# Kernel tuning notes

Hardware: AMD Instinct MI355X
Metric: run time of the kernel (lower is better)

## Reference

```python
import jax, jax.numpy as jnp
import numpy as np

SIZE = 32          # resize target (self.size)
WIN = 11           # SSIM gaussian window
SIGMA = 1.5
THRESH = 0.3       # cal_thresh
C1 = (0.01 * 255.0) ** 2
C2 = (0.03 * 255.0) ** 2


def _gauss_kernel():
    x = jnp.arange(WIN, dtype=jnp.float32) - (WIN - 1) / 2.0
    g = jnp.exp(-(x ** 2) / (2.0 * SIGMA ** 2))
    g = g / g.sum()
    k = jnp.outer(g, g)
    return jnp.tile(k[None, None], (3, 1, 1, 1))  # [3,1,11,11] depthwise


def _dwconv(x, k):
    # x: [N,3,h,w] depthwise gaussian blur, SAME padding (pytorch-ssim style)
    return jax.lax.conv_general_dilated(x, k, (1, 1), 'SAME', feature_group_count=3)


def _crop_resize(img, box, H, W):
    # img [3,H,W], box cxcywh -> [3,SIZE,SIZE]; mimics int() crop + F.interpolate
    # (bilinear, align_corners=False)
    cx, cy, w, h = box[0], box[1], box[2], box[3]
    x0 = jnp.clip(jnp.floor(cx - w / 2), 0.0, W - 1.0)
    x1 = jnp.clip(jnp.floor(cx + w / 2), 0.0, float(W))
    y0 = jnp.clip(jnp.floor(cy - h / 2), 0.0, H - 1.0)
    y1 = jnp.clip(jnp.floor(cy + h / 2), 0.0, float(H))
    wp = jnp.maximum(x1 - x0, 1.0)  # crop width (>=1 to stay well-defined)
    hp = jnp.maximum(y1 - y0, 1.0)
    d = jnp.arange(SIZE, dtype=jnp.float32) + 0.5
    sx = x0 + jnp.clip(d * wp / SIZE - 0.5, 0.0, wp - 1.0)  # source cols
    sy = y0 + jnp.clip(d * hp / SIZE - 0.5, 0.0, hp - 1.0)  # source rows
    ix0 = jnp.floor(sx); iy0 = jnp.floor(sy)
    fx = sx - ix0; fy = sy - iy0
    ix0 = ix0.astype(jnp.int32); iy0 = iy0.astype(jnp.int32)
    ix1 = jnp.minimum(ix0 + 1, (x0 + wp - 1.0).astype(jnp.int32))
    iy1 = jnp.minimum(iy0 + 1, (y0 + hp - 1.0).astype(jnp.int32))

    def gat(iy, ix):
        return img[:, iy[:, None], ix[None, :]]  # [3,SIZE,SIZE]

    return (gat(iy0, ix0) * ((1 - fy)[None, :, None] * (1 - fx)[None, None, :])
            + gat(iy0, ix1) * ((1 - fy)[None, :, None] * fx[None, None, :])
            + gat(iy1, ix0) * (fy[None, :, None] * (1 - fx)[None, None, :])
            + gat(iy1, ix1) * (fy[None, :, None] * fx[None, None, :]))


def _pairwise_iou(gt, pr, eps=1e-16):
    # gt [B,Ng,4], pr [B,Np,4] cxcywh -> iou [B,Ng,Np] (same math as get_two_box_iou)
    g1, g2 = gt[:, :, None, :2], gt[:, :, None, 2:]
    p1, p2 = pr[:, None, :, :2], pr[:, None, :, 2:]
    tl = jnp.maximum(g1 - g2 / 2, p1 - p2 / 2)
    br = jnp.minimum(g1 + g2 / 2, p1 + p2 / 2)
    a_g = jnp.prod(gt[:, :, 2:], -1)[:, :, None]
    a_p = jnp.prod(pr[:, :, 2:], -1)[:, None, :]
    en = jnp.prod((tl < br).astype(gt.dtype), -1)
    a_i = jnp.prod(br - tl, -1) * en
    return a_i / (a_g + a_p - a_i + eps)


def _forward(imgs, gt_boxes, pred_boxes):
    B, C, H, W = imgs.shape
    Ng, Np = gt_boxes.shape[1], pred_boxes.shape[1]
    iou = _pairwise_iou(gt_boxes, pred_boxes)                        # [B,Ng,Np]
    valid = ((iou > THRESH)
             & (pred_boxes[:, None, :, 2] > 2)
             & (pred_boxes[:, None, :, 3] > 2))
    crop = jax.vmap(lambda im, bx: jax.vmap(lambda b: _crop_resize(im, b, H, W))(bx))
    g = crop(imgs, gt_boxes)    # [B,Ng,3,32,32]
    p = crop(imgs, pred_boxes)  # [B,Np,3,32,32]

    k = _gauss_kernel()
    mu_g = _dwconv(g.reshape(B * Ng, 3, SIZE, SIZE), k).reshape(B, Ng, 3, SIZE, SIZE)
    mu_p = _dwconv(p.reshape(B * Np, 3, SIZE, SIZE), k).reshape(B, Np, 3, SIZE, SIZE)
    sig_g = _dwconv((g * g).reshape(B * Ng, 3, SIZE, SIZE), k).reshape(B, Ng, 3, SIZE, SIZE) - mu_g ** 2
    sig_p = _dwconv((p * p).reshape(B * Np, 3, SIZE, SIZE), k).reshape(B, Np, 3, SIZE, SIZE) - mu_p ** 2

    gp = g[:, :, None] * p[:, None, :]                               # [B,Ng,Np,3,32,32]
    mug = mu_g[:, :, None]; mup = mu_p[:, None, :]
    sig_gp = _dwconv(gp.reshape(B * Ng * Np, 3, SIZE, SIZE), k).reshape(B, Ng, Np, 3, SIZE, SIZE) - mug * mup
    ssim_map = ((2 * mug * mup + C1) * (2 * sig_gp + C2)) / ((mug ** 2 + mup ** 2 + C1) * (sig_g[:, :, None] + sig_p[:, None, :] + C2))
    ssim_pair = ssim_map.mean(axis=(-3, -2, -1))                     # [B,Ng,Np]

    l1_pair = (jnp.abs(g[:, :, None] - p[:, None, :]) / 255.0).mean(axis=(-3, -2, -1))

    wv = valid.astype(imgs.dtype)
    cnt = wv.sum()
    mean_valid = lambda x: (x * wv).sum() / jnp.maximum(cnt, 1.0)
    # original: (L1(p/255,g/255) + SSIM_loss(p,g)).mean() over valid pairs
    loss = mean_valid(l1_pair) + (1.0 - mean_valid(ssim_pair))
    return jnp.where(cnt > 0, loss, jnp.zeros((), imgs.dtype))


def setup_inputs() -> dict:
    key = jax.random.key(0)
    k1, k2, k3, k4 = jax.random.split(key, 4)
    B, H, W, Ng, Np = 4, 640, 640, 16, 64
    imgs = jax.random.uniform(k1, (B, 3, H, W), jnp.float32, 0.0, 255.0)
    cxy = jax.random.uniform(k2, (B, Ng, 2), jnp.float32, 64.0, 576.0)
    wh = jax.random.uniform(k3, (B, Ng, 2), jnp.float32, 16.0, 128.0)
    gt_boxes = jnp.concatenate([cxy, wh], -1)
    # preds = jittered copies of GT so many pairs pass the IoU > 0.3 gate
    pred_boxes = jnp.tile(gt_boxes, (1, Np // Ng, 1)) + jax.random.normal(k4, (B, Np, 4), jnp.float32) * 4.0
    return {"imgs": imgs, "gt_boxes": gt_boxes, "pred_boxes": pred_boxes}


def reference(imgs, gt_boxes, pred_boxes):
    return _forward(imgs, gt_boxes, pred_boxes)
```

## Files before the change

kernel.cpp:

```cpp
#include <hip/hip_runtime.h>
#include <math.h>

#define WIN 11
#define HALF 5
#define SZ 32
#define PST 33
#define BB 4
#define NG 16
#define NP 64
#define IH 640
#define IW 640
#define CPIX 1024
#define NPIX 3072
#define NCROP 320
#define NPAIR 4096
#define NSLOT 512
#define SSIM_C1 6.5025f
#define SSIM_C2 58.5225f

#define GW_INIT {0.001028379f, 0.007598757f, 0.036000791f, 0.109360748f, \
                 0.213005174f, 0.266011868f, 0.213005174f, 0.109360748f, \
                 0.036000791f, 0.007598757f, 0.001028379f}


__global__ __launch_bounds__(256) void k_crop_valid(const float* __restrict__ imgs,
                                                    const float* __restrict__ gt,
                                                    const float* __restrict__ pr,
                                                    float* __restrict__ crops,
                                                    float* __restrict__ mus,
                                                    float* __restrict__ sigs,
                                                    int* __restrict__ list,
                                                    int* __restrict__ count) {
    const int blk = blockIdx.x;
    const int t = threadIdx.x;

    if (blk == 3 * NCROP) {
        __shared__ int s_wcnt[4];
        __shared__ int s_base;
        const int wave = t >> 6, lane = t & 63;
        if (t == 0) s_base = 0;
#pragma unroll 1
        for (int iter = 0; iter < NPAIR / 256; ++iter) {
            int idx = iter * 256 + t;
            int b = idx >> 10;
            int r = idx & 1023;
            int gi = r >> 6, pi = r & 63;
            const float* g = gt + (b * NG + gi) * 4;
            const float* p = pr + (b * NP + pi) * 4;
            float gx = g[0], gy = g[1], gw = g[2], gh = g[3];
            float px = p[0], py = p[1], pw = p[2], ph = p[3];
            float tlx = fmaxf(gx - gw * 0.5f, px - pw * 0.5f);
            float tly = fmaxf(gy - gh * 0.5f, py - ph * 0.5f);
            float brx = fminf(gx + gw * 0.5f, px + pw * 0.5f);
            float bry = fminf(gy + gh * 0.5f, py + ph * 0.5f);
            float en = ((tlx < brx) && (tly < bry)) ? 1.f : 0.f;
            float ai = (brx - tlx) * (bry - tly) * en;
            float iou = ai / (gw * gh + pw * ph - ai + 1e-16f);
            bool valid = (iou > 0.3f && pw > 2.f && ph > 2.f);
            unsigned long long m = __ballot(valid);
            if (lane == 0) s_wcnt[wave] = __popcll(m);
            __syncthreads();
            int base = s_base;
            int woff = base;
#pragma unroll
            for (int w = 0; w < 4; ++w)
                if (w < wave) woff += s_wcnt[w];
            int sum = s_wcnt[0] + s_wcnt[1] + s_wcnt[2] + s_wcnt[3];
            if (valid) {
                int pos = woff + __popcll(m & ((1ull << lane) - 1ull));
                list[pos] = idx;
            }
            __syncthreads();
            if (t == 0) s_base = base + sum;
        }
        __syncthreads();
        if (t == 0) *count = s_base;
        return;
    }

    const int crop = blk / 3;
    const int c = blk - crop * 3;
    int b;
    const float* box;
    if (crop < BB * NG) {
        b = crop >> 4;
        box = gt + crop * 4;
    } else {
        int id = crop - BB * NG;
        b = id >> 6;
        box = pr + id * 4;
    }

    __shared__ float cr[SZ][PST];
    __shared__ float t1[SZ][PST];
    __shared__ float t2[SZ][PST];

    float cx = box[0], cy = box[1], bw = box[2], bh = box[3];
    float x0 = fminf(fmaxf(floorf(cx - bw * 0.5f), 0.f), (float)(IW - 1));
    float x1 = fminf(fmaxf(floorf(cx + bw * 0.5f), 0.f), (float)IW);
    float y0 = fminf(fmaxf(floorf(cy - bh * 0.5f), 0.f), (float)(IH - 1));
    float y1 = fminf(fmaxf(floorf(cy + bh * 0.5f), 0.f), (float)IH);
    float wp = fmaxf(x1 - x0, 1.f);
    float hp = fmaxf(y1 - y0, 1.f);
    int xmax = (int)(x0 + wp - 1.f);
    int ymax = (int)(y0 + hp - 1.f);

    const int y = t >> 3;
    const int xb = (t & 7) * 4;

    float sy = y0 + fminf(fmaxf(((float)y + 0.5f) * hp * (1.f / 32.f) - 0.5f, 0.f), hp - 1.f);
    float fly = floorf(sy);
    int iy0 = (int)fly;
    float fy = sy - fly;
    int iy1 = min(iy0 + 1, ymax);

    const float* ic = imgs + ((size_t)b * 3 + c) * IH * IW;
    const float* r0 = ic + iy0 * IW;
    const float* r1 = ic + iy1 * IW;
    float vv[4];
#pragma unroll
    for (int j = 0; j < 4; ++j) {
        int x = xb + j;
        float sx = x0 + fminf(fmaxf(((float)x + 0.5f) * wp * (1.f / 32.f) - 0.5f, 0.f), wp - 1.f);
        float flx = floorf(sx);
        int ix0 = (int)flx;
        float fx = sx - flx;
        int ix1 = min(ix0 + 1, xmax);
        float v00 = r0[ix0], v01 = r0[ix1], v10 = r1[ix0], v11 = r1[ix1];
        float v = v00 * (1.f - fy) * (1.f - fx) + v01 * (1.f - fy) * fx +
                  v10 * fy * (1.f - fx) + v11 * fy * fx;
        vv[j] = v;
        cr[y][x] = v;
    }
    float* dst = crops + (size_t)crop * NPIX + c * CPIX + t * 4;
    *(float4*)dst = make_float4(vv[0], vv[1], vv[2], vv[3]);
    __syncthreads();

    constexpr float GW[WIN] = GW_INIT;
#pragma unroll
    for (int j = 0; j < 4; ++j) {
        int x = xb + j;
        float a1 = 0.f, a2 = 0.f;
#pragma unroll
        for (int k = 0; k < WIN; ++k) {
            int xx = x + k - HALF;
            if (xx >= 0 && xx < SZ) {
                float v = cr[y][xx];
                a1 += GW[k] * v;
                a2 += GW[k] * v * v;
            }
        }
        t1[y][x] = a1;
        t2[y][x] = a2;
    }
    __syncthreads();
    float m[4], s[4];
#pragma unroll
    for (int j = 0; j < 4; ++j) {
        int x = xb + j;
        float a1 = 0.f, a2 = 0.f;
#pragma unroll
        for (int k = 0; k < WIN; ++k) {
            int yy = y + k - HALF;
            if (yy >= 0 && yy < SZ) {
                a1 += GW[k] * t1[yy][x];
                a2 += GW[k] * t2[yy][x];
            }
        }
        m[j] = a1;
        s[j] = a2 - a1 * a1;
    }
    float* mdst = mus + (size_t)crop * NPIX + c * CPIX + t * 4;
    float* sdst = sigs + (size_t)crop * NPIX + c * CPIX + t * 4;
    *(float4*)mdst = make_float4(m[0], m[1], m[2], m[3]);
    *(float4*)sdst = make_float4(s[0], s[1], s[2], s[3]);
}

__global__ __launch_bounds__(256) void k_pair(const int* __restrict__ list,
                                              const int* __restrict__ count,
                                              const float* __restrict__ crops,
                                              const float* __restrict__ mus,
                                              const float* __restrict__ sigs,
                                              float* __restrict__ pairL1,
                                              float* __restrict__ pairSS) {
    const int c = blockIdx.x;
    const int n = *count;
    const int t = threadIdx.x;
    const int y = t >> 3;
    const int xb = (t & 7) * 4;
    const int wave = t >> 6, lane = t & 63;

    __shared__ float gp[SZ][PST];
    __shared__ float tmp[SZ][PST];
    __shared__ float rl[4], rs[4];
    constexpr float GW[WIN] = GW_INIT;

    for (int slot = blockIdx.y; slot < n; slot += NSLOT) {
        const int pair = list[slot];
        const int b = pair >> 10;
        const int r = pair & 1023;
        const int gi = r >> 6, pi = r & 63;
        const size_t goff = (size_t)(b * NG + gi) * NPIX + c * CPIX;
        const size_t poff = (size_t)(BB * NG + b * NP + pi) * NPIX + c * CPIX;

        float4 gv = *(const float4*)(crops + goff + t * 4);
        float4 pv = *(const float4*)(crops + poff + t * 4);
        float4 mg = *(const float4*)(mus + goff + t * 4);
        float4 mp = *(const float4*)(mus + poff + t * 4);
        float4 sg = *(const float4*)(sigs + goff + t * 4);
        float4 sp = *(const float4*)(sigs + poff + t * 4);

        float l1 = fabsf(gv.x - pv.x) + fabsf(gv.y - pv.y) +
                   fabsf(gv.z - pv.z) + fabsf(gv.w - pv.w);
        gp[y][xb + 0] = gv.x * pv.x;
        gp[y][xb + 1] = gv.y * pv.y;
        gp[y][xb + 2] = gv.z * pv.z;
        gp[y][xb + 3] = gv.w * pv.w;
        __syncthreads();

#pragma unroll
        for (int j = 0; j < 4; ++j) {
            int x = xb + j;
            float a = 0.f;
#pragma unroll
            for (int k = 0; k < WIN; ++k) {
                int xx = x + k - HALF;
                if (xx >= 0 && xx < SZ) a += GW[k] * gp[y][xx];
            }
            tmp[y][x] = a;
        }
        __syncthreads();

        float mgv[4] = {mg.x, mg.y, mg.z, mg.w};
        float mpv[4] = {mp.x, mp.y, mp.z, mp.w};
        float sgv[4] = {sg.x, sg.y, sg.z, sg.w};
        float spv[4] = {sp.x, sp.y, sp.z, sp.w};
        float ss = 0.f;
#pragma unroll
        for (int j = 0; j < 4; ++j) {
            int x = xb + j;
            float a = 0.f;
#pragma unroll
            for (int k = 0; k < WIN; ++k) {
                int yy = y + k - HALF;
                if (yy >= 0 && yy < SZ) a += GW[k] * tmp[yy][x];
            }
            float m1 = mgv[j], m2 = mpv[j];
            float sgp = a - m1 * m2;
            float num = (2.f * m1 * m2 + SSIM_C1) * (2.f * sgp + SSIM_C2);
            float den = (m1 * m1 + m2 * m2 + SSIM_C1) * (sgv[j] + spv[j] + SSIM_C2);
            ss += num / den;
        }

#pragma unroll
        for (int off = 32; off > 0; off >>= 1) {
            l1 += __shfl_down(l1, off);
            ss += __shfl_down(ss, off);
        }
        if (lane == 0) { rl[wave] = l1; rs[wave] = ss; }
        __syncthreads();
        if (t == 0) {
            pairL1[slot * 3 + c] = rl[0] + rl[1] + rl[2] + rl[3];
            pairSS[slot * 3 + c] = rs[0] + rs[1] + rs[2] + rs[3];
        }
    }
}

__global__ __launch_bounds__(256) void k_final(const int* __restrict__ count,
                                               const float* __restrict__ pairL1,
                                               const float* __restrict__ pairSS,
                                               float* __restrict__ out) {
    const int n3 = (*count) * 3;
    const int t = threadIdx.x;
    float L = 0.f, S = 0.f;
    for (int i = t; i < n3; i += 256) {
        L += pairL1[i];
        S += pairSS[i];
    }
    __shared__ float rl[4], rs[4];
#pragma unroll
    for (int off = 32; off > 0; off >>= 1) {
        L += __shfl_down(L, off);
        S += __shfl_down(S, off);
    }
    const int wave = t >> 6, lane = t & 63;
    if (lane == 0) { rl[wave] = L; rs[wave] = S; }
    __syncthreads();
    if (t == 0) {
        float cnt = (float)(*count);
        float Lt = (rl[0] + rl[1] + rl[2] + rl[3]) * (1.0f / (255.0f * (float)NPIX));
        float St = (rs[0] + rs[1] + rs[2] + rs[3]) * (1.0f / (float)NPIX);
        float m = fmaxf(cnt, 1.f);
        float loss = Lt / m + 1.f - St / m;
        out[0] = (cnt > 0.f) ? loss : 0.f;
    }
}

extern "C" void kernel_launch(void* const* d_in, const int* in_sizes, int n_in,
                              void* d_out, int out_size, void* d_ws, size_t ws_size,
                              hipStream_t stream) {
    const float* imgs = (const float*)d_in[0];
    const float* gt = (const float*)d_in[1];
    const float* pr = (const float*)d_in[2];

    float* ws = (float*)d_ws;
    float* crops = ws;
    float* mus = crops + (size_t)NCROP * NPIX;
    float* sigs = mus + (size_t)NCROP * NPIX;
    float* pairL1 = sigs + (size_t)NCROP * NPIX;
    float* pairSS = pairL1 + (size_t)NPAIR * 3;
    int* list = (int*)(pairSS + (size_t)NPAIR * 3);
    int* count = list + NPAIR;

    k_crop_valid<<<3 * NCROP + 1, 256, 0, stream>>>(imgs, gt, pr, crops, mus, sigs,
                                                    list, count);
    k_pair<<<dim3(3, NSLOT), 256, 0, stream>>>(list, count, crops, mus, sigs,
                                               pairL1, pairSS);
    k_final<<<1, 256, 0, stream>>>(count, pairL1, pairSS, (float*)d_out);
}
```

Baseline: 88.45 us.

## Fuse crop resampling and blur statistics into per-pair kernel, drop workspace crops

```diff
diff --git a/kernel.cpp b/kernel.cpp
--- a/kernel.cpp
+++ b/kernel.cpp
@@ -10,9 +10,7 @@
 #define NP 64
 #define IH 640
 #define IW 640
-#define CPIX 1024
 #define NPIX 3072
-#define NCROP 320
 #define NPAIR 4096
 #define NSLOT 512
 #define SSIM_C1 6.5025f
@@ -23,78 +21,62 @@
                  0.036000791f, 0.007598757f, 0.001028379f}
 
 
-__global__ __launch_bounds__(256) void k_crop_valid(const float* __restrict__ imgs,
-                                                    const float* __restrict__ gt,
-                                                    const float* __restrict__ pr,
-                                                    float* __restrict__ crops,
-                                                    float* __restrict__ mus,
-                                                    float* __restrict__ sigs,
-                                                    int* __restrict__ list,
-                                                    int* __restrict__ count) {
-    const int blk = blockIdx.x;
+__device__ __forceinline__ bool pair_valid(const float* __restrict__ gt,
+                                           const float* __restrict__ pr, int idx) {
+    int b = idx >> 10;
+    int r = idx & 1023;
+    int gi = r >> 6, pi = r & 63;
+    const float* g = gt + (b * NG + gi) * 4;
+    const float* p = pr + (b * NP + pi) * 4;
+    float gx = g[0], gy = g[1], gw = g[2], gh = g[3];
+    float px = p[0], py = p[1], pw = p[2], ph = p[3];
+    float tlx = fmaxf(gx - gw * 0.5f, px - pw * 0.5f);
+    float tly = fmaxf(gy - gh * 0.5f, py - ph * 0.5f);
+    float brx = fminf(gx + gw * 0.5f, px + pw * 0.5f);
+    float bry = fminf(gy + gh * 0.5f, py + ph * 0.5f);
+    float en = ((tlx < brx) && (tly < bry)) ? 1.f : 0.f;
+    float ai = (brx - tlx) * (bry - tly) * en;
+    float iou = ai / (gw * gh + pw * ph - ai + 1e-16f);
+    return (iou > 0.3f && pw > 2.f && ph > 2.f);
+}
+
+__global__ __launch_bounds__(256) void k_valid(const float* __restrict__ gt,
+                                               const float* __restrict__ pr,
+                                               int* __restrict__ list,
+                                               int* __restrict__ count) {
     const int t = threadIdx.x;
-
-    if (blk == 3 * NCROP) {
-        __shared__ int s_wcnt[4];
-        __shared__ int s_base;
-        const int wave = t >> 6, lane = t & 63;
-        if (t == 0) s_base = 0;
+    const int wave = t >> 6, lane = t & 63;
+    __shared__ int s_wcnt[4];
+
+    int cnt = 0;
 #pragma unroll 1
-        for (int iter = 0; iter < NPAIR / 256; ++iter) {
-            int idx = iter * 256 + t;
-            int b = idx >> 10;
-            int r = idx & 1023;
-            int gi = r >> 6, pi = r & 63;
-            const float* g = gt + (b * NG + gi) * 4;
-            const float* p = pr + (b * NP + pi) * 4;
-            float gx = g[0], gy = g[1], gw = g[2], gh = g[3];
-            float px = p[0], py = p[1], pw = p[2], ph = p[3];
-            float tlx = fmaxf(gx - gw * 0.5f, px - pw * 0.5f);
-            float tly = fmaxf(gy - gh * 0.5f, py - ph * 0.5f);
-            float brx = fminf(gx + gw * 0.5f, px + pw * 0.5f);
-            float bry = fminf(gy + gh * 0.5f, py + ph * 0.5f);
-            float en = ((tlx < brx) && (tly < bry)) ? 1.f : 0.f;
-            float ai = (brx - tlx) * (bry - tly) * en;
-            float iou = ai / (gw * gh + pw * ph - ai + 1e-16f);
-            bool valid = (iou > 0.3f && pw > 2.f && ph > 2.f);
-            unsigned long long m = __ballot(valid);
-            if (lane == 0) s_wcnt[wave] = __popcll(m);
-            __syncthreads();
-            int base = s_base;
-            int woff = base;
-#pragma unroll
-            for (int w = 0; w < 4; ++w)
-                if (w < wave) woff += s_wcnt[w];
-            int sum = s_wcnt[0] + s_wcnt[1] + s_wcnt[2] + s_wcnt[3];
-            if (valid) {
-                int pos = woff + __popcll(m & ((1ull << lane) - 1ull));
-                list[pos] = idx;
-            }
-            __syncthreads();
-            if (t == 0) s_base = base + sum;
-        }
-        __syncthreads();
-        if (t == 0) *count = s_base;
-        return;
-    }
-
-    const int crop = blk / 3;
-    const int c = blk - crop * 3;
-    int b;
-    const float* box;
-    if (crop < BB * NG) {
-        b = crop >> 4;
-        box = gt + crop * 4;
-    } else {
-        int id = crop - BB * NG;
-        b = id >> 6;
-        box = pr + id * 4;
-    }
-
-    __shared__ float cr[SZ][PST];
-    __shared__ float t1[SZ][PST];
-    __shared__ float t2[SZ][PST];
-
+    for (int i = 0; i < 16; ++i) {
+        int idx = wave * 1024 + i * 64 + lane;
+        unsigned long long m = __ballot(pair_valid(gt, pr, idx));
+        cnt += __popcll(m);
+    }
+    if (lane == 0) s_wcnt[wave] = cnt;
+    __syncthreads();
+
+    int base = 0;
+#pragma unroll
+    for (int w = 0; w < 4; ++w)
+        if (w < wave) base += s_wcnt[w];
+
+#pragma unroll 1
+    for (int i = 0; i < 16; ++i) {
+        int idx = wave * 1024 + i * 64 + lane;
+        bool v = pair_valid(gt, pr, idx);
+        unsigned long long m = __ballot(v);
+        if (v) list[base + __popcll(m & ((1ull << lane) - 1ull))] = idx;
+        base += __popcll(m);
+    }
+    if (t == 0) *count = s_wcnt[0] + s_wcnt[1] + s_wcnt[2] + s_wcnt[3];
+}
+
+__device__ __forceinline__ void bilinear4(const float* __restrict__ ic,
+                                          const float* __restrict__ box,
+                                          int y, int xb, float out[4]) {
     float cx = box[0], cy = box[1], bw = box[2], bh = box[3];
     float x0 = fminf(fmaxf(floorf(cx - bw * 0.5f), 0.f), (float)(IW - 1));
     float x1 = fminf(fmaxf(floorf(cx + bw * 0.5f), 0.f), (float)IW);
@@ -105,19 +87,13 @@
     int xmax = (int)(x0 + wp - 1.f);
     int ymax = (int)(y0 + hp - 1.f);
 
-    const int y = t >> 3;
-    const int xb = (t & 7) * 4;
-
     float sy = y0 + fminf(fmaxf(((float)y + 0.5f) * hp * (1.f / 32.f) - 0.5f, 0.f), hp - 1.f);
     float fly = floorf(sy);
     int iy0 = (int)fly;
     float fy = sy - fly;
     int iy1 = min(iy0 + 1, ymax);
-
-    const float* ic = imgs + ((size_t)b * 3 + c) * IH * IW;
     const float* r0 = ic + iy0 * IW;
     const float* r1 = ic + iy1 * IW;
-    float vv[4];
 #pragma unroll
     for (int j = 0; j < 4; ++j) {
         int x = xb + j;
@@ -127,62 +103,18 @@
         float fx = sx - flx;
         int ix1 = min(ix0 + 1, xmax);
         float v00 = r0[ix0], v01 = r0[ix1], v10 = r1[ix0], v11 = r1[ix1];
-        float v = v00 * (1.f - fy) * (1.f - fx) + v01 * (1.f - fy) * fx +
-                  v10 * fy * (1.f - fx) + v11 * fy * fx;
-        vv[j] = v;
-        cr[y][x] = v;
-    }
-    float* dst = crops + (size_t)crop * NPIX + c * CPIX + t * 4;
-    *(float4*)dst = make_float4(vv[0], vv[1], vv[2], vv[3]);
-    __syncthreads();
-
-    constexpr float GW[WIN] = GW_INIT;
-#pragma unroll
-    for (int j = 0; j < 4; ++j) {
-        int x = xb + j;
-        float a1 = 0.f, a2 = 0.f;
-#pragma unroll
-        for (int k = 0; k < WIN; ++k) {
-            int xx = x + k - HALF;
-            if (xx >= 0 && xx < SZ) {
-                float v = cr[y][xx];
-                a1 += GW[k] * v;
-                a2 += GW[k] * v * v;
-            }
-        }
-        t1[y][x] = a1;
-        t2[y][x] = a2;
-    }
-    __syncthreads();
-    float m[4], s[4];
-#pragma unroll
-    for (int j = 0; j < 4; ++j) {
-        int x = xb + j;
-        float a1 = 0.f, a2 = 0.f;
-#pragma unroll
-        for (int k = 0; k < WIN; ++k) {
-            int yy = y + k - HALF;
-            if (yy >= 0 && yy < SZ) {
-                a1 += GW[k] * t1[yy][x];
-                a2 += GW[k] * t2[yy][x];
-            }
-        }
-        m[j] = a1;
-        s[j] = a2 - a1 * a1;
-    }
-    float* mdst = mus + (size_t)crop * NPIX + c * CPIX + t * 4;
-    float* sdst = sigs + (size_t)crop * NPIX + c * CPIX + t * 4;
-    *(float4*)mdst = make_float4(m[0], m[1], m[2], m[3]);
-    *(float4*)sdst = make_float4(s[0], s[1], s[2], s[3]);
-}
-
-__global__ __launch_bounds__(256) void k_pair(const int* __restrict__ list,
-                                              const int* __restrict__ count,
-                                              const float* __restrict__ crops,
-                                              const float* __restrict__ mus,
-                                              const float* __restrict__ sigs,
-                                              float* __restrict__ pairL1,
-                                              float* __restrict__ pairSS) {
+        out[j] = v00 * (1.f - fy) * (1.f - fx) + v01 * (1.f - fy) * fx +
+                 v10 * fy * (1.f - fx) + v11 * fy * fx;
+    }
+}
+
+__global__ __launch_bounds__(256) void k_all(const int* __restrict__ list,
+                                             const int* __restrict__ count,
+                                             const float* __restrict__ imgs,
+                                             const float* __restrict__ gt,
+                                             const float* __restrict__ pr,
+                                             float* __restrict__ pairL1,
+                                             float* __restrict__ pairSS) {
     const int c = blockIdx.x;
     const int n = *count;
     const int t = threadIdx.x;
@@ -190,8 +122,13 @@
     const int xb = (t & 7) * 4;
     const int wave = t >> 6, lane = t & 63;
 
-    __shared__ float gp[SZ][PST];
-    __shared__ float tmp[SZ][PST];
+    __shared__ float cg[SZ][PST];
+    __shared__ float cp[SZ][PST];
+    __shared__ float hg[SZ][PST];
+    __shared__ float hg2[SZ][PST];
+    __shared__ float hp_[SZ][PST];
+    __shared__ float hp2[SZ][PST];
+    __shared__ float hgp[SZ][PST];
     __shared__ float rl[4], rs[4];
     constexpr float GW[WIN] = GW_INIT;
 
@@ -200,55 +137,70 @@
         const int b = pair >> 10;
         const int r = pair & 1023;
         const int gi = r >> 6, pi = r & 63;
-        const size_t goff = (size_t)(b * NG + gi) * NPIX + c * CPIX;
-        const size_t poff = (size_t)(BB * NG + b * NP + pi) * NPIX + c * CPIX;
-
-        float4 gv = *(const float4*)(crops + goff + t * 4);
-        float4 pv = *(const float4*)(crops + poff + t * 4);
-        float4 mg = *(const float4*)(mus + goff + t * 4);
-        float4 mp = *(const float4*)(mus + poff + t * 4);
-        float4 sg = *(const float4*)(sigs + goff + t * 4);
-        float4 sp = *(const float4*)(sigs + poff + t * 4);
-
-        float l1 = fabsf(gv.x - pv.x) + fabsf(gv.y - pv.y) +
-                   fabsf(gv.z - pv.z) + fabsf(gv.w - pv.w);
-        gp[y][xb + 0] = gv.x * pv.x;
-        gp[y][xb + 1] = gv.y * pv.y;
-        gp[y][xb + 2] = gv.z * pv.z;
-        gp[y][xb + 3] = gv.w * pv.w;
+        const float* gbox = gt + (b * NG + gi) * 4;
+        const float* pbox = pr + (b * NP + pi) * 4;
+        const float* ic = imgs + ((size_t)b * 3 + c) * IH * IW;
+
+        float gv[4], pv[4];
+        bilinear4(ic, gbox, y, xb, gv);
+        bilinear4(ic, pbox, y, xb, pv);
+
+        float l1 = 0.f;
+#pragma unroll
+        for (int j = 0; j < 4; ++j) {
+            l1 += fabsf(gv[j] - pv[j]);
+            cg[y][xb + j] = gv[j];
+            cp[y][xb + j] = pv[j];
+        }
         __syncthreads();
 
 #pragma unroll
         for (int j = 0; j < 4; ++j) {
             int x = xb + j;
-            float a = 0.f;
+            float a1 = 0.f, a2 = 0.f, a3 = 0.f, a4 = 0.f, a5 = 0.f;
 #pragma unroll
             for (int k = 0; k < WIN; ++k) {
                 int xx = x + k - HALF;
-                if (xx >= 0 && xx < SZ) a += GW[k] * gp[y][xx];
+                if (xx >= 0 && xx < SZ) {
+                    float gval = cg[y][xx];
+                    float pval = cp[y][xx];
+                    a1 += GW[k] * gval;
+                    a2 += GW[k] * gval * gval;
+                    a3 += GW[k] * pval;
+                    a4 += GW[k] * pval * pval;
+                    a5 += GW[k] * gval * pval;
+                }
             }
-            tmp[y][x] = a;
+            hg[y][x] = a1;
+            hg2[y][x] = a2;
+            hp_[y][x] = a3;
+            hp2[y][x] = a4;
+            hgp[y][x] = a5;
         }
         __syncthreads();
 
-        float mgv[4] = {mg.x, mg.y, mg.z, mg.w};
-        float mpv[4] = {mp.x, mp.y, mp.z, mp.w};
-        float sgv[4] = {sg.x, sg.y, sg.z, sg.w};
-        float spv[4] = {sp.x, sp.y, sp.z, sp.w};
         float ss = 0.f;
 #pragma unroll
         for (int j = 0; j < 4; ++j) {
             int x = xb + j;
-            float a = 0.f;
+            float a1 = 0.f, a2 = 0.f, a3 = 0.f, a4 = 0.f, a5 = 0.f;
 #pragma unroll
             for (int k = 0; k < WIN; ++k) {
                 int yy = y + k - HALF;
-                if (yy >= 0 && yy < SZ) a += GW[k] * tmp[yy][x];
+                if (yy >= 0 && yy < SZ) {
+                    a1 += GW[k] * hg[yy][x];
+                    a2 += GW[k] * hg2[yy][x];
+                    a3 += GW[k] * hp_[yy][x];
+                    a4 += GW[k] * hp2[yy][x];
+                    a5 += GW[k] * hgp[yy][x];
+                }
             }
-            float m1 = mgv[j], m2 = mpv[j];
-            float sgp = a - m1 * m2;
+            float m1 = a1, m2 = a3;
+            float sg = a2 - m1 * m1;
+            float sp = a4 - m2 * m2;
+            float sgp = a5 - m1 * m2;
             float num = (2.f * m1 * m2 + SSIM_C1) * (2.f * sgp + SSIM_C2);
-            float den = (m1 * m1 + m2 * m2 + SSIM_C1) * (sgv[j] + spv[j] + SSIM_C2);
+            float den = (m1 * m1 + m2 * m2 + SSIM_C1) * (sg + sp + SSIM_C2);
             ss += num / den;
         }
 
@@ -304,17 +256,12 @@
     const float* pr = (const float*)d_in[2];
 
     float* ws = (float*)d_ws;
-    float* crops = ws;
-    float* mus = crops + (size_t)NCROP * NPIX;
-    float* sigs = mus + (size_t)NCROP * NPIX;
-    float* pairL1 = sigs + (size_t)NCROP * NPIX;
+    float* pairL1 = ws;
     float* pairSS = pairL1 + (size_t)NPAIR * 3;
     int* list = (int*)(pairSS + (size_t)NPAIR * 3);
     int* count = list + NPAIR;
 
-    k_crop_valid<<<3 * NCROP + 1, 256, 0, stream>>>(imgs, gt, pr, crops, mus, sigs,
-                                                    list, count);
-    k_pair<<<dim3(3, NSLOT), 256, 0, stream>>>(list, count, crops, mus, sigs,
-                                               pairL1, pairSS);
+    k_valid<<<1, 256, 0, stream>>>(gt, pr, list, count);
+    k_all<<<dim3(3, NSLOT), 256, 0, stream>>>(list, count, imgs, gt, pr, pairL1, pairSS);
     k_final<<<1, 256, 0, stream>>>(count, pairL1, pairSS, (float*)d_out);
 }
```

Result: slower. 97.01 us (+9.7%).

## Use per-wave two-pass pair compaction and paired float2 loads for bilinear gather

Applied to the files above, without the earlier changes.

```diff
diff --git a/kernel.cpp b/kernel.cpp
--- a/kernel.cpp
+++ b/kernel.cpp
@@ -23,6 +23,25 @@
                  0.036000791f, 0.007598757f, 0.001028379f}
 
 
+__device__ __forceinline__ bool pair_valid(const float* __restrict__ gt,
+                                           const float* __restrict__ pr, int idx) {
+    int b = idx >> 10;
+    int r = idx & 1023;
+    int gi = r >> 6, pi = r & 63;
+    const float* g = gt + (b * NG + gi) * 4;
+    const float* p = pr + (b * NP + pi) * 4;
+    float gx = g[0], gy = g[1], gw = g[2], gh = g[3];
+    float px = p[0], py = p[1], pw = p[2], ph = p[3];
+    float tlx = fmaxf(gx - gw * 0.5f, px - pw * 0.5f);
+    float tly = fmaxf(gy - gh * 0.5f, py - ph * 0.5f);
+    float brx = fminf(gx + gw * 0.5f, px + pw * 0.5f);
+    float bry = fminf(gy + gh * 0.5f, py + ph * 0.5f);
+    float en = ((tlx < brx) && (tly < bry)) ? 1.f : 0.f;
+    float ai = (brx - tlx) * (bry - tly) * en;
+    float iou = ai / (gw * gh + pw * ph - ai + 1e-16f);
+    return (iou > 0.3f && pw > 2.f && ph > 2.f);
+}
+
 __global__ __launch_bounds__(256) void k_crop_valid(const float* __restrict__ imgs,
                                                     const float* __restrict__ gt,
                                                     const float* __restrict__ pr,
@@ -33,48 +52,31 @@
                                                     int* __restrict__ count) {
     const int blk = blockIdx.x;
     const int t = threadIdx.x;
+    const int wave = t >> 6, lane = t & 63;
 
     if (blk == 3 * NCROP) {
         __shared__ int s_wcnt[4];
-        __shared__ int s_base;
-        const int wave = t >> 6, lane = t & 63;
-        if (t == 0) s_base = 0;
+        int cnt = 0;
 #pragma unroll 1
-        for (int iter = 0; iter < NPAIR / 256; ++iter) {
-            int idx = iter * 256 + t;
-            int b = idx >> 10;
-            int r = idx & 1023;
-            int gi = r >> 6, pi = r & 63;
-            const float* g = gt + (b * NG + gi) * 4;
-            const float* p = pr + (b * NP + pi) * 4;
-            float gx = g[0], gy = g[1], gw = g[2], gh = g[3];
-            float px = p[0], py = p[1], pw = p[2], ph = p[3];
-            float tlx = fmaxf(gx - gw * 0.5f, px - pw * 0.5f);
-            float tly = fmaxf(gy - gh * 0.5f, py - ph * 0.5f);
-            float brx = fminf(gx + gw * 0.5f, px + pw * 0.5f);
-            float bry = fminf(gy + gh * 0.5f, py + ph * 0.5f);
-            float en = ((tlx < brx) && (tly < bry)) ? 1.f : 0.f;
-            float ai = (brx - tlx) * (bry - tly) * en;
-            float iou = ai / (gw * gh + pw * ph - ai + 1e-16f);
-            bool valid = (iou > 0.3f && pw > 2.f && ph > 2.f);
-            unsigned long long m = __ballot(valid);
-            if (lane == 0) s_wcnt[wave] = __popcll(m);
-            __syncthreads();
-            int base = s_base;
-            int woff = base;
-#pragma unroll
-            for (int w = 0; w < 4; ++w)
-                if (w < wave) woff += s_wcnt[w];
-            int sum = s_wcnt[0] + s_wcnt[1] + s_wcnt[2] + s_wcnt[3];
-            if (valid) {
-                int pos = woff + __popcll(m & ((1ull << lane) - 1ull));
-                list[pos] = idx;
-            }
-            __syncthreads();
-            if (t == 0) s_base = base + sum;
-        }
+        for (int i = 0; i < 16; ++i) {
+            unsigned long long m = __ballot(pair_valid(gt, pr, wave * 1024 + i * 64 + lane));
+            cnt += __popcll(m);
+        }
+        if (lane == 0) s_wcnt[wave] = cnt;
         __syncthreads();
-        if (t == 0) *count = s_base;
+        int base = 0;
+#pragma unroll
+        for (int w = 0; w < 4; ++w)
+            if (w < wave) base += s_wcnt[w];
+#pragma unroll 1
+        for (int i = 0; i < 16; ++i) {
+            int idx = wave * 1024 + i * 64 + lane;
+            bool v = pair_valid(gt, pr, idx);
+            unsigned long long m = __ballot(v);
+            if (v) list[base + __popcll(m & ((1ull << lane) - 1ull))] = idx;
+            base += __popcll(m);
+        }
+        if (t == 0) *count = s_wcnt[0] + s_wcnt[1] + s_wcnt[2] + s_wcnt[3];
         return;
     }
 
@@ -125,12 +127,17 @@
         float flx = floorf(sx);
         int ix0 = (int)flx;
         float fx = sx - flx;
-        int ix1 = min(ix0 + 1, xmax);
-        float v00 = r0[ix0], v01 = r0[ix1], v10 = r1[ix0], v11 = r1[ix1];
-        float v = v00 * (1.f - fy) * (1.f - fx) + v01 * (1.f - fy) * fx +
-                  v10 * fy * (1.f - fx) + v11 * fy * fx;
-        vv[j] = v;
-        cr[y][x] = v;
+        int ixb = max(min(ix0, xmax - 1), 0);
+        bool cl = (ix0 > ixb);
+        float2 q0 = *(const float2*)(r0 + ixb);
+        float2 q1 = *(const float2*)(r1 + ixb);
+        float v00 = cl ? q0.y : q0.x;
+        float v01 = q0.y;
+        float v10 = cl ? q1.y : q1.x;
+        float v11 = q1.y;
+        vv[j] = v00 * (1.f - fy) * (1.f - fx) + v01 * (1.f - fy) * fx +
+                v10 * fy * (1.f - fx) + v11 * fy * fx;
+        cr[y][x] = vv[j];
     }
     float* dst = crops + (size_t)crop * NPIX + c * CPIX + t * 4;
     *(float4*)dst = make_float4(vv[0], vv[1], vv[2], vv[3]);
```

New measurement: 87.75 us (median of 2 runs). About the same (-0.8%).
